# Optimization experiments

Measured on AMD Instinct MI355X. Metric: run time of the kernel, lower is better.

Reference implementation:

```python
import jax, jax.numpy as jnp
import numpy as np


def l2norm(t, eps=1e-12):
    # matches F.normalize(p=2, dim=-1): divide by norm clamped to eps
    n = jnp.linalg.norm(t, axis=-1, keepdims=True)
    return t / jnp.maximum(n, eps)


def setup_inputs() -> dict:
    key = jax.random.key(0)
    kx, ke = jax.random.split(key)
    B, N, D, C = 8, 1024, 256, 8192
    x = jax.random.normal(kx, (B, N, D), dtype=jnp.float32)
    # codebook initialized l2-normalized, as in __init__ (kmeans_init=False)
    embed = l2norm(jax.random.normal(ke, (1, C, D), dtype=jnp.float32))
    return {"x": x, "embed": embed}


def reference(x, embed):
    # x: [B, N, D]; ndim < 4 -> add codebook dim h=1
    xh = x[None]                                   # [1, B, N, D]
    h, b, n, d = xh.shape
    flat = l2norm(xh.reshape(h, b * n, d))         # [1, B*N, D]
    e = l2norm(embed)                              # [1, C, D]
    # cosine-similarity distances
    dist = jnp.einsum('hnd,hcd->hnc', flat, e)     # [1, B*N, C]
    # sample_codebook_temp == 0 -> plain argmax
    idx = jnp.argmax(dist, axis=-1).reshape(h, b, n)  # [1, B, N]
    # batched_embedding: gather UN-normalized codebook rows
    quantize = jax.vmap(lambda em, ix: em[ix])(embed, idx)  # [1, B, N, D]
    # needs_codebook_dim -> strip leading dim
    return quantize[0], idx[0]
```

## Files before the change

kernel.cpp:

```cpp
#include <hip/hip_runtime.h>
#include <math.h>

#define QROWS 8192
#define DDIM  256
#define CCNT  8192

typedef __attribute__((ext_vector_type(4))) float f32x4;
typedef __attribute__((ext_vector_type(8))) short bf16x8;

__device__ __forceinline__ unsigned short f2bf(float f) {
    unsigned u = __float_as_uint(f);
    u += 0x7fffu + ((u >> 16) & 1u);
    return (unsigned short)(u >> 16);
}
__device__ __forceinline__ unsigned u32max(unsigned a, unsigned b) { return a > b ? a : b; }
__device__ __forceinline__ unsigned u32min(unsigned a, unsigned b) { return a < b ? a : b; }

__device__ __forceinline__ unsigned key32(float v, unsigned enc) {
    unsigned u = __float_as_uint(v);
    unsigned s = (unsigned)((int)u >> 31);
    return ((u ^ (s | 0x80000000u)) & 0xFFFFFF00u) | enc;
}

__global__ void k_prep(const float* __restrict__ x, unsigned short* __restrict__ xb,
                       const float* __restrict__ e, unsigned short* __restrict__ eb) {
    const int bid = blockIdx.x;
    if (bid < 1024) {
        const int i = (bid * 256 + threadIdx.x) * 8;
        const float4 f0 = *reinterpret_cast<const float4*>(x + i);
        const float4 f1 = *reinterpret_cast<const float4*>(x + i + 4);
        uint4 o;
        o.x = f2bf(f0.x) | ((unsigned)f2bf(f0.y) << 16);
        o.y = f2bf(f0.z) | ((unsigned)f2bf(f0.w) << 16);
        o.z = f2bf(f1.x) | ((unsigned)f2bf(f1.y) << 16);
        o.w = f2bf(f1.z) | ((unsigned)f2bf(f1.w) << 16);
        *reinterpret_cast<uint4*>(xb + i) = o;
    } else {
        const int row  = (bid - 1024) * 4 + (threadIdx.x >> 6);
        const int lane = threadIdx.x & 63;
        const float4 v = *reinterpret_cast<const float4*>(e + (size_t)row * DDIM + lane * 4);
        float s = v.x * v.x + v.y * v.y + v.z * v.z + v.w * v.w;
        #pragma unroll
        for (int off = 1; off < 64; off <<= 1) s += __shfl_xor(s, off);
        const float inv = 1.0f / fmaxf(sqrtf(s), 1e-12f);
        ushort4 o;
        o.x = f2bf(v.x * inv); o.y = f2bf(v.y * inv);
        o.z = f2bf(v.z * inv); o.w = f2bf(v.w * inv);
        *reinterpret_cast<ushort4*>(eb + (size_t)row * DDIM + lane * 4) = o;
    }
}

#define GLOAD_LDS(g, s) \
    __builtin_amdgcn_global_load_lds((const __attribute__((address_space(1))) void*)(g), \
                                     (__attribute__((address_space(3))) void*)(s), 16, 0, 0)

#define SBAR do { asm volatile("" ::: "memory"); __builtin_amdgcn_s_barrier(); \
                  asm volatile("" ::: "memory"); } while (0)
#define WAIT_LGKM(n) do { asm volatile("s_waitcnt lgkmcnt(" #n ")" ::: "memory"); \
                          __builtin_amdgcn_sched_barrier(0); } while (0)
#define WAIT_VM(n) do { asm volatile("s_waitcnt vmcnt(" #n ")" ::: "memory"); \
                        __builtin_amdgcn_sched_barrier(0); } while (0)

__launch_bounds__(512, 2)
__global__ void k_gemm(const unsigned short* __restrict__ xb,
                       const unsigned short* __restrict__ eb,
                       unsigned* pout ) {
    extern __shared__ char smem[];

    const int tid = threadIdx.x;
    const int w = tid >> 6, l = tid & 63;
    const int lg = l >> 4, lr = l & 15, lr7 = lr & 7;
    const int bid = blockIdx.x;
    const int panel = (bid & 7) * 2 + ((bid >> 3) >> 4);
    const int split = (bid >> 3) & 15;
    const int n0 = panel * 512, c0 = split * 512;

    const int lchk = (tid & 24) | ((tid & 7) ^ ((tid >> 5) & 7));
    const char* baseA = (const char*)xb + (size_t)(n0 + (tid >> 5)) * 512 + lchk * 16;
    const char* baseB = (const char*)eb + (size_t)(c0 + (tid >> 5)) * 512 + lchk * 16;
    const int wl16 = w * 1024;

#define STAGE_AHALF(h) do { _Pragma("unroll") for (int g_ = 0; g_ < 16; ++g_)              \
    GLOAD_LDS(baseA + (h) * 131072 + g_ * 8192, smem + g_ * 8192 + wl16); } while (0)
#define STAGEB(t) do { _Pragma("unroll") for (int g_ = 0; g_ < 2; ++g_)                    \
    GLOAD_LDS(baseB + (size_t)(t) * 16384 + g_ * 8192,                                     \
              smem + ((t) & 7) * 16384 + g_ * 8192 + wl16); } while (0)

    bf16x8 aF[4][8];
#define READA() do { _Pragma("unroll") for (int mi_ = 0; mi_ < 4; ++mi_)                   \
    _Pragma("unroll") for (int kk_ = 0; kk_ < 8; ++kk_) {                                  \
        const int lc_ = kk_ * 4 + lg;                                                      \
        const int ph_ = (lc_ & 24) | ((lc_ & 7) ^ lr7);                                    \
        aF[mi_][kk_] = *reinterpret_cast<const bf16x8*>(                                   \
            smem + ((w & 3) * 64 + mi_ * 16 + lr) * 512 + ph_ * 16); } } while (0)

    STAGE_AHALF(0);
    WAIT_VM(0); SBAR;
    if (w < 4) READA();
    WAIT_LGKM(0); SBAR;
    STAGE_AHALF(1);
    WAIT_VM(0); SBAR;
    if (w >= 4) READA();
    WAIT_LGKM(0); SBAR;
    STAGEB(0); STAGEB(1); STAGEB(2); STAGEB(3); STAGEB(4); STAGEB(5);

    const f32x4 zf4 = {0.f, 0.f, 0.f, 0.f};
    f32x4 acc[4][2];
    unsigned rk1[16], rk2[16];
    #pragma unroll
    for (int i = 0; i < 16; ++i) { rk1[i] = 0u; rk2[i] = 0u; }

#define TILE(t) do {                                                                       \
    const char* sb_ = smem + ((t) & 7) * 16384;                                            \
    _Pragma("unroll") for (int mi_ = 0; mi_ < 4; ++mi_)                                    \
        { acc[mi_][0] = zf4; acc[mi_][1] = zf4; }                                          \
    _Pragma("unroll") for (int kk_ = 0; kk_ < 8; ++kk_) {                                  \
        const int lc_ = kk_ * 4 + lg;                                                      \
        const int ph_ = ((lc_ & 24) | ((lc_ & 7) ^ lr7)) * 16;                             \
        const bf16x8 b0_ = *reinterpret_cast<const bf16x8*>(sb_ + (lr) * 512 + ph_);       \
        const bf16x8 b1_ = *reinterpret_cast<const bf16x8*>(sb_ + (16 + lr) * 512 + ph_);  \
        _Pragma("unroll") for (int mi_ = 0; mi_ < 4; ++mi_) {                              \
            acc[mi_][0] = __builtin_amdgcn_mfma_f32_16x16x32_bf16(aF[mi_][kk_], b0_, acc[mi_][0], 0, 0, 0); \
            acc[mi_][1] = __builtin_amdgcn_mfma_f32_16x16x32_bf16(aF[mi_][kk_], b1_, acc[mi_][1], 0, 0, 0); \
        } }                                                                                \
    const unsigned encb_ = (unsigned)(255 - ((t) & 7) * 32) - (unsigned)lr;                \
    _Pragma("unroll") for (int mi_ = 0; mi_ < 4; ++mi_)                                    \
        _Pragma("unroll") for (int rr_ = 0; rr_ < 4; ++rr_) {                              \
            const unsigned q0_ = key32(acc[mi_][0][rr_], encb_);                           \
            const unsigned q1_ = key32(acc[mi_][1][rr_], encb_ - 16u);                     \
            const unsigned m01_ = u32max(q0_, q1_), n01_ = u32min(q0_, q1_);               \
            const int i_ = mi_ * 4 + rr_;                                                  \
            const unsigned lo_ = u32min(rk1[i_], m01_);                                    \
            rk1[i_] = u32max(rk1[i_], m01_);                                               \
            rk2[i_] = u32max(u32max(rk2[i_], n01_), lo_);                                  \
        }                                                                                  \
} while (0)

#define FLUSH(half) do {                                                                   \
    _Pragma("unroll") for (int i_ = 0; i_ < 16; ++i_) {                                    \
        unsigned t1_ = rk1[i_], t2_ = rk2[i_];                                             \
        _Pragma("unroll") for (int off_ = 1; off_ < 16; off_ <<= 1) {                      \
            const unsigned o1_ = __shfl_xor(t1_, off_);                                    \
            const unsigned o2_ = __shfl_xor(t2_, off_);                                    \
            const unsigned n1_ = u32max(t1_, o1_), lo_ = u32min(t1_, o1_);                 \
            t2_ = u32max(u32max(t2_, o2_), lo_);                                           \
            t1_ = n1_;                                                                     \
        }                                                                                  \
        if (lr == 0) {                                                                     \
            const int row_ = n0 + w * 64 + (i_ >> 2) * 16 + lg * 4 + (i_ & 3);             \
            uint2 o_; o_.x = t1_; o_.y = t2_;                                              \
            *reinterpret_cast<uint2*>(pout + (size_t)row_ * 256 + split * 4 + (half) * 2) = o_; \
        }                                                                                  \
        rk1[i_] = 0u; rk2[i_] = 0u;                                                        \
    }                                                                                      \
} while (0)

    #pragma unroll 1
    for (int u = 0; u < 8; ++u) {
        if (u < 6)       { WAIT_VM(8); }
        else if (u == 6) { WAIT_VM(4); }
        else             { WAIT_VM(0); }
        SBAR;
        if (u < 5) { STAGEB(2 * u + 6); STAGEB(2 * u + 7); }
        TILE(2 * u);
        TILE(2 * u + 1);
        if (u == 3) FLUSH(0);
        if (u == 7) FLUSH(1);
    }
#undef STAGE_AHALF
#undef STAGEB
#undef READA
#undef TILE
#undef FLUSH
}

__global__ void k_fixup(const unsigned* pk,
                        const float* __restrict__ x, const float* __restrict__ e,
                        float* out) {
    const int row = blockIdx.x * 4 + (threadIdx.x >> 6);
    const int t   = threadIdx.x & 63;
    unsigned long long kk0 = 0ull, kk1 = 0ull;
    if (t < 32) {
        const uint2 kv = reinterpret_cast<const uint2*>(pk + (size_t)row * 256)[t];
        const int col0 = t * 256 + 255 - (int)(kv.x & 255u);
        kk0 = ((unsigned long long)(kv.x & 0xFFFFFF00u) << 32) | (unsigned)(~col0);
        const int col1 = t * 256 + 255 - (int)(kv.y & 255u);
        kk1 = ((unsigned long long)(kv.y & 0xFFFFFF00u) << 32) | (unsigned)(~col1);
    }

    int cand[4];
    #pragma unroll
    for (int p = 0; p < 4; ++p) {
        unsigned long long m = kk0 > kk1 ? kk0 : kk1;
        #pragma unroll
        for (int off = 1; off < 64; off <<= 1) {
            const unsigned long long o = __shfl_xor(m, off);
            if (o > m) m = o;
        }
        cand[p] = (int)(~(unsigned)m) & (CCNT - 1);
        if (kk0 == m) kk0 = 0ull;
        if (kk1 == m) kk1 = 0ull;
    }

    const float4 xv = *reinterpret_cast<const float4*>(x + (size_t)row * DDIM + t * 4);
    float best = -INFINITY; int bc = 0x7fffffff;
    #pragma unroll
    for (int p = 0; p < 4; ++p) {
        const int c = cand[p];
        const float4 ev = *reinterpret_cast<const float4*>(e + (size_t)c * DDIM + t * 4);
        float d  = xv.x * ev.x + xv.y * ev.y + xv.z * ev.z + xv.w * ev.w;
        float ss = ev.x * ev.x + ev.y * ev.y + ev.z * ev.z + ev.w * ev.w;
        #pragma unroll
        for (int off = 1; off < 64; off <<= 1) {
            d  += __shfl_xor(d, off);
            ss += __shfl_xor(ss, off);
        }
        const float v = d * (1.0f / fmaxf(sqrtf(ss), 1e-12f));
        if (v > best || (v == best && c < bc)) { best = v; bc = c; }
    }

    if (t == 0) out[(size_t)QROWS * DDIM + row] = (float)bc;
    const float4 q = *reinterpret_cast<const float4*>(e + (size_t)bc * DDIM + t * 4);
    *reinterpret_cast<float4*>(out + (size_t)row * DDIM + t * 4) = q;
}

extern "C" void kernel_launch(void* const* d_in, const int* in_sizes, int n_in,
                              void* d_out, int out_size, void* d_ws, size_t ws_size,
                              hipStream_t stream) {
    const float* x = (const float*)d_in[0];
    const float* e = (const float*)d_in[1];
    float* out = (float*)d_out;
    char* ws = (char*)d_ws;

    unsigned short* xb = (unsigned short*)ws;
    unsigned short* eb = (unsigned short*)(ws + (size_t)4 * 1024 * 1024);

    hipFuncSetAttribute(reinterpret_cast<const void*>(k_gemm),
                        hipFuncAttributeMaxDynamicSharedMemorySize, 131072);

    k_prep<<<3072, 256, 0, stream>>>(x, xb, e, eb);
    k_gemm<<<256, 512, 131072, stream>>>(xb, eb, (unsigned*)d_out);
    k_fixup<<<QROWS / 4, 256, 0, stream>>>((const unsigned*)d_out, x, e, out);
}
```

Measured before the change: 60.27 us.

## Deepen B-tile prefetch to 8 stages and process 4 tiles per barrier

The B-tile staging schedule changes. All 8 shared-memory slots are prefetched up front, and each loop iteration processes four tiles with a single barrier, refilling four slots in a batch instead of two. The first MFMA of each tile takes a zero accumulator directly, so the separate zero-initialisation goes away. The argmax key encoding also drops the sign-dependent bit flip, which assumes the top similarity scores are non-negative. Coarser refill batches may expose more load latency at the stage boundaries, and negative scores would now order incorrectly.

```diff
diff --git a/kernel.cpp b/kernel.cpp
--- a/kernel.cpp
+++ b/kernel.cpp
@@ -17,9 +17,7 @@
 __device__ __forceinline__ unsigned u32min(unsigned a, unsigned b) { return a < b ? a : b; }
 
 __device__ __forceinline__ unsigned key32(float v, unsigned enc) {
-    unsigned u = __float_as_uint(v);
-    unsigned s = (unsigned)((int)u >> 31);
-    return ((u ^ (s | 0x80000000u)) & 0xFFFFFF00u) | enc;
+    return ((__float_as_uint(v) ^ 0x80000000u) & 0xFFFFFF00u) | enc;
 }
 
 __global__ void k_prep(const float* __restrict__ x, unsigned short* __restrict__ xb,
@@ -102,37 +100,46 @@
     WAIT_VM(0); SBAR;
     if (w >= 4) READA();
     WAIT_LGKM(0); SBAR;
-    STAGEB(0); STAGEB(1); STAGEB(2); STAGEB(3); STAGEB(4); STAGEB(5);
+    STAGEB(0); STAGEB(1); STAGEB(2); STAGEB(3);
+    STAGEB(4); STAGEB(5); STAGEB(6); STAGEB(7);
 
     const f32x4 zf4 = {0.f, 0.f, 0.f, 0.f};
-    f32x4 acc[4][2];
     unsigned rk1[16], rk2[16];
     #pragma unroll
     for (int i = 0; i < 16; ++i) { rk1[i] = 0u; rk2[i] = 0u; }
 
 #define TILE(t) do {                                                                       \
     const char* sb_ = smem + ((t) & 7) * 16384;                                            \
-    _Pragma("unroll") for (int mi_ = 0; mi_ < 4; ++mi_)                                    \
-        { acc[mi_][0] = zf4; acc[mi_][1] = zf4; }                                          \
-    _Pragma("unroll") for (int kk_ = 0; kk_ < 8; ++kk_) {                                  \
+    f32x4 ac0_[4], ac1_[4];                                                                \
+    {                                                                                      \
+        const int ph0_ = ((lg & 24) | ((lg & 7) ^ lr7)) * 16;                              \
+        const bf16x8 b0_ = *reinterpret_cast<const bf16x8*>(sb_ + lr * 512 + ph0_);        \
+        const bf16x8 b1_ = *reinterpret_cast<const bf16x8*>(sb_ + (16 + lr) * 512 + ph0_); \
+        _Pragma("unroll") for (int mi_ = 0; mi_ < 4; ++mi_) {                              \
+            ac0_[mi_] = __builtin_amdgcn_mfma_f32_16x16x32_bf16(aF[mi_][0], b0_, zf4, 0, 0, 0); \
+            ac1_[mi_] = __builtin_amdgcn_mfma_f32_16x16x32_bf16(aF[mi_][0], b1_, zf4, 0, 0, 0); \
+        }                                                                                  \
+    }                                                                                      \
+    _Pragma("unroll") for (int kk_ = 1; kk_ < 8; ++kk_) {                                  \
         const int lc_ = kk_ * 4 + lg;                                                      \
         const int ph_ = ((lc_ & 24) | ((lc_ & 7) ^ lr7)) * 16;                             \
-        const bf16x8 b0_ = *reinterpret_cast<const bf16x8*>(sb_ + (lr) * 512 + ph_);       \
+        const bf16x8 b0_ = *reinterpret_cast<const bf16x8*>(sb_ + lr * 512 + ph_);         \
         const bf16x8 b1_ = *reinterpret_cast<const bf16x8*>(sb_ + (16 + lr) * 512 + ph_);  \
         _Pragma("unroll") for (int mi_ = 0; mi_ < 4; ++mi_) {                              \
-            acc[mi_][0] = __builtin_amdgcn_mfma_f32_16x16x32_bf16(aF[mi_][kk_], b0_, acc[mi_][0], 0, 0, 0); \
-            acc[mi_][1] = __builtin_amdgcn_mfma_f32_16x16x32_bf16(aF[mi_][kk_], b1_, acc[mi_][1], 0, 0, 0); \
-        } }                                                                                \
+            ac0_[mi_] = __builtin_amdgcn_mfma_f32_16x16x32_bf16(aF[mi_][kk_], b0_, ac0_[mi_], 0, 0, 0); \
+            ac1_[mi_] = __builtin_amdgcn_mfma_f32_16x16x32_bf16(aF[mi_][kk_], b1_, ac1_[mi_], 0, 0, 0); \
+        }                                                                                  \
+    }                                                                                      \
     const unsigned encb_ = (unsigned)(255 - ((t) & 7) * 32) - (unsigned)lr;                \
     _Pragma("unroll") for (int mi_ = 0; mi_ < 4; ++mi_)                                    \
         _Pragma("unroll") for (int rr_ = 0; rr_ < 4; ++rr_) {                              \
-            const unsigned q0_ = key32(acc[mi_][0][rr_], encb_);                           \
-            const unsigned q1_ = key32(acc[mi_][1][rr_], encb_ - 16u);                     \
+            const unsigned q0_ = key32(ac0_[mi_][rr_], encb_);                             \
+            const unsigned q1_ = key32(ac1_[mi_][rr_], encb_ - 16u);                       \
             const unsigned m01_ = u32max(q0_, q1_), n01_ = u32min(q0_, q1_);               \
             const int i_ = mi_ * 4 + rr_;                                                  \
             const unsigned lo_ = u32min(rk1[i_], m01_);                                    \
             rk1[i_] = u32max(rk1[i_], m01_);                                               \
-            rk2[i_] = u32max(u32max(rk2[i_], n01_), lo_);                                  \
+            rk2[i_] = u32max(rk2[i_], u32max(n01_, lo_));                                  \
         }                                                                                  \
 } while (0)
 
@@ -156,16 +163,20 @@
 } while (0)
 
     #pragma unroll 1
-    for (int u = 0; u < 8; ++u) {
-        if (u < 6)       { WAIT_VM(8); }
-        else if (u == 6) { WAIT_VM(4); }
+    for (int u = 0; u < 4; ++u) {
+        if (u == 0)      { WAIT_VM(8); }
+        else if (u == 1) { WAIT_VM(0); }
+        else if (u == 2) { WAIT_VM(16); }
         else             { WAIT_VM(0); }
         SBAR;
-        if (u < 5) { STAGEB(2 * u + 6); STAGEB(2 * u + 7); }
-        TILE(2 * u);
-        TILE(2 * u + 1);
-        if (u == 3) FLUSH(0);
-        if (u == 7) FLUSH(1);
+        if (u == 1) { STAGEB(8); STAGEB(9); STAGEB(10); STAGEB(11); }
+        if (u == 2) { STAGEB(12); STAGEB(13); STAGEB(14); STAGEB(15); }
+        TILE(4 * u);
+        TILE(4 * u + 1);
+        TILE(4 * u + 2);
+        TILE(4 * u + 3);
+        if (u == 1) FLUSH(0);
+        if (u == 3) FLUSH(1);
     }
 #undef STAGE_AHALF
 #undef STAGEB
```

Result: slower. 74.52 us (+23.6%).
